# Performance work log

Measured on AMD Instinct MI355X. Metric: run time of the kernel, lower is better.

## Reference

```python
import jax, jax.numpy as jnp
import numpy as np

NUM_GROUPS = 32
EPS = 1e-6


def group_norm(x, gamma, beta):
    # x: [b, c, t, h, w]
    b, c, t, h, w = x.shape
    xg = x.reshape(b, NUM_GROUPS, c // NUM_GROUPS, t, h, w)
    mean = xg.mean(axis=(2, 3, 4, 5), keepdims=True)
    var = xg.var(axis=(2, 3, 4, 5), keepdims=True)
    xg = (xg - mean) * jax.lax.rsqrt(var + EPS)
    xn = xg.reshape(b, c, t, h, w)
    return xn * gamma[None, :, None, None, None] + beta[None, :, None, None, None]


def conv1x1(x, w, bias):
    # 1x1x1 Conv3d == per-position channel matmul. x: [b,c,t,h,w], w: [cout,cin]
    y = jnp.einsum('oc,bcthw->bothw', w, x)
    return y + bias[None, :, None, None, None]


def setup_inputs() -> dict:
    key = jax.random.key(0)
    ks = jax.random.split(key, 11)
    c = 512
    b, t, h, w = 1, 16, 32, 32
    s = 1.0 / np.sqrt(c)
    return {
        'x': jax.random.normal(ks[0], (b, c, t, h, w), dtype=jnp.float32),
        'gn_gamma': jnp.ones((c,), jnp.float32),
        'gn_beta': jnp.zeros((c,), jnp.float32),
        'wq': jax.random.normal(ks[1], (c, c), jnp.float32) * s,
        'bq': jnp.zeros((c,), jnp.float32),
        'wk': jax.random.normal(ks[2], (c, c), jnp.float32) * s,
        'bk': jnp.zeros((c,), jnp.float32),
        'wv': jax.random.normal(ks[3], (c, c), jnp.float32) * s,
        'bv': jnp.zeros((c,), jnp.float32),
        'wo': jax.random.normal(ks[4], (c, c), jnp.float32) * s,
        'bo': jnp.zeros((c,), jnp.float32),
    }


def reference(x, gn_gamma, gn_beta, wq, bq, wk, bk, wv, bv, wo, bo):
    b, c, t, h, w = x.shape
    h_ = group_norm(x, gn_gamma, gn_beta)
    q = conv1x1(h_, wq, bq)
    k = conv1x1(h_, wk, bk)
    v = conv1x1(h_, wv, bv)
    # per-frame spatial attention: tokens are the h*w grid, batched over (b t)
    n = h * w
    q = q.transpose(0, 2, 3, 4, 1).reshape(b * t, n, c)   # [(bt), n, c]
    k = k.transpose(0, 2, 3, 4, 1).reshape(b * t, n, c)
    v = v.transpose(0, 2, 3, 4, 1).reshape(b * t, n, c)
    scale = float(int(c) ** (-0.5))
    attn = jax.nn.softmax(jnp.einsum('bic,bjc->bij', q, k) * scale, axis=-1)
    out = jnp.einsum('bij,bjc->bic', attn, v)             # [(bt), n, c]
    out = out.reshape(b, t, h, w, c).transpose(0, 4, 1, 2, 3)
    out = conv1x1(out, wo, bo)
    return x + out
```

## Files before the change

kernel.cpp:

```cpp
#include <hip/hip_runtime.h>
#include <hip/hip_bf16.h>

#define CCH   512
#define NPOS  16384
#define NTOK  1024
#define NFRM  16
#define NGRP  32
#define GSZ   (CCH / NGRP)
#define GELEM (GSZ * NPOS)
#define GN_SPLIT 32

typedef unsigned short u16;
typedef unsigned int   u32;
typedef __attribute__((ext_vector_type(8))) short  short8;
typedef __attribute__((ext_vector_type(4))) float  floatx4;

__device__ __forceinline__ float bf2f(u16 u) {
    return __uint_as_float(((u32)u) << 16);
}
__device__ __forceinline__ u16 f2bf(float f) {
    u32 u = __float_as_uint(f);
    u = (u + 0x7fffu + ((u >> 16) & 1u)) >> 16;
    return (u16)u;
}
__device__ __forceinline__ float ldx(const void* p, size_t i, bool f32m) {
    return f32m ? ((const float*)p)[i] : bf2f(((const u16*)p)[i]);
}
__device__ __forceinline__ void gl2lds16(const u16* g, u16* l) {
    __builtin_amdgcn_global_load_lds(
        (const __attribute__((address_space(1))) u32*)g,
        (__attribute__((address_space(3))) u32*)l, 16, 0, 0);
}

__launch_bounds__(256)
__global__ void detect_dtype(const u32* __restrict__ x32, u32* __restrict__ flag) {
    __shared__ int cnt;
    if (threadIdx.x == 0) cnt = 0;
    __syncthreads();
    int c = 0;
    for (int i = threadIdx.x; i < 4096; i += 256) {
        u32 v = x32[i] & 0xFFFFu;
        u32 e = (v >> 7) & 0xFFu;
        if (e >= 0xC8u) c++;
    }
    atomicAdd(&cnt, c);
    __syncthreads();
    if (threadIdx.x == 0) *flag = (cnt > 64) ? 1u : 0u;
}

__launch_bounds__(256)
__global__ void conv_all(const void* w0, const void* w1, const void* w2, const void* w3,
                         const void* b0, const void* b1, const void* b2, const void* b3,
                         u16* __restrict__ wdst, u16* __restrict__ bdst,
                         float* __restrict__ rl,
                         const u32* __restrict__ flag) {
    int b = blockIdx.x;
    if (b > 1024) {
        rl[(b - 1025) * 256 + threadIdx.x] = 0.0f;
        return;
    }
    bool f32m = *flag != 0u;
    if (b < 1024) {
        int wi = b >> 8;
        const void* src = (wi == 0) ? w0 : (wi == 1) ? w1 : (wi == 2) ? w2 : w3;
        int base = (b & 255) * 1024 + threadIdx.x * 4;
        u16* d = wdst + wi * 262144 + base;
        if (f32m) {
            float4 v = *(const float4*)((const float*)src + base);
            ushort4 o;
            o.x = f2bf(v.x); o.y = f2bf(v.y); o.z = f2bf(v.z); o.w = f2bf(v.w);
            *(ushort4*)d = o;
        } else {
            *(ushort4*)d = *(const ushort4*)((const u16*)src + base);
        }
    } else {
        int t = threadIdx.x;
        int bi = t >> 6;
        int off = (t & 63) * 8;
        const void* src = (bi == 0) ? b0 : (bi == 1) ? b1 : (bi == 2) ? b2 : b3;
        u16* d = bdst + bi * 512 + off;
        if (f32m) {
            float4 v1 = *(const float4*)((const float*)src + off);
            float4 v2 = *(const float4*)((const float*)src + off + 4);
            ushort4 o1, o2;
            o1.x = f2bf(v1.x); o1.y = f2bf(v1.y); o1.z = f2bf(v1.z); o1.w = f2bf(v1.w);
            o2.x = f2bf(v2.x); o2.y = f2bf(v2.y); o2.z = f2bf(v2.z); o2.w = f2bf(v2.w);
            *(ushort4*)d = o1; *(ushort4*)(d + 4) = o2;
        } else {
            *(ushort4*)d = *(const ushort4*)((const u16*)src + off);
            *(ushort4*)(d + 4) = *(const ushort4*)((const u16*)src + off + 4);
        }
    }
}

__launch_bounds__(256)
__global__ void gn_partial(const void* __restrict__ x, float2* __restrict__ partials,
                           const u32* __restrict__ flag) {
    __shared__ float sm[8];
    bool f32m = *flag != 0u;
    const int chunk = GELEM / GN_SPLIT;
    size_t base = (size_t)blockIdx.x * chunk;
    float s = 0.f, ss = 0.f;
    if (f32m) {
        const float4* p = (const float4*)((const float*)x + base);
        for (int i = threadIdx.x; i < chunk / 4; i += 256) {
            float4 u = p[i];
            s  += u.x + u.y + u.z + u.w;
            ss += u.x * u.x + u.y * u.y + u.z * u.z + u.w * u.w;
        }
    } else {
        const ushort4* p = (const ushort4*)((const u16*)x + base);
        for (int i = threadIdx.x; i < chunk / 4; i += 256) {
            ushort4 u = p[i];
            float a = bf2f(u.x), b = bf2f(u.y), c = bf2f(u.z), d = bf2f(u.w);
            s  += a + b + c + d;
            ss += a * a + b * b + c * c + d * d;
        }
    }
    int lane = threadIdx.x & 63, w = threadIdx.x >> 6;
    float t = s;
    #pragma unroll
    for (int o = 32; o > 0; o >>= 1) t += __shfl_down(t, o, 64);
    if (lane == 0) sm[w] = t;
    t = ss;
    #pragma unroll
    for (int o = 32; o > 0; o >>= 1) t += __shfl_down(t, o, 64);
    if (lane == 0) sm[4 + w] = t;
    __syncthreads();
    if (threadIdx.x == 0)
        partials[blockIdx.x] = make_float2(sm[0] + sm[1] + sm[2] + sm[3],
                                           sm[4] + sm[5] + sm[6] + sm[7]);
}

__launch_bounds__(256)
__global__ void gn_coef(const float2* __restrict__ partials, const void* __restrict__ gamma,
                        const void* __restrict__ beta, float2* __restrict__ coef,
                        const u32* __restrict__ flag) {
    bool f32m = *flag != 0u;
    int c = blockIdx.x * 256 + threadIdx.x;
    if (c < CCH) {
        int g = c >> 4;
        float sum = 0.f, sq = 0.f;
        #pragma unroll
        for (int i = 0; i < GN_SPLIT; ++i) {
            float2 p = partials[g * GN_SPLIT + i];
            sum += p.x; sq += p.y;
        }
        float mean = sum * (1.0f / (float)GELEM);
        float var  = fmaxf(sq * (1.0f / (float)GELEM) - mean * mean, 0.0f);
        float rstd = rsqrtf(var + 1e-6f);
        float gm = ldx(gamma, c, f32m), b = ldx(beta, c, f32m);
        float sc = rstd * gm;
        coef[c] = make_float2(sc, b - mean * sc);
    }
}

__launch_bounds__(256)
__global__ void gn_apply_t(const void* __restrict__ x, const float2* __restrict__ coef,
                           u16* __restrict__ xt, const u32* __restrict__ flag) {
    bool f32m = *flag != 0u;
    __shared__ float tile[64][65];
    int p0 = blockIdx.x * 64, c0 = blockIdx.y * 64;
    int lane = threadIdx.x & 63, rg = threadIdx.x >> 6;
    #pragma unroll 4
    for (int i = 0; i < 16; ++i) {
        int row = rg * 16 + i;
        int c = c0 + row;
        float2 cf = coef[c];
        float v = ldx(x, (size_t)c * NPOS + p0 + lane, f32m);
        tile[row][lane] = v * cf.x + cf.y;
    }
    __syncthreads();
    #pragma unroll 4
    for (int i = 0; i < 16; ++i) {
        int prow = rg * 16 + i;
        xt[(size_t)(p0 + prow) * CCH + c0 + lane] = f2bf(tile[lane][prow]);
    }
}

#define EPI_QK    0
#define EPI_V     1
#define EPI_SCEXP 2
#define EPI_PV    3
#define EPI_OUT   4

template<int EPI, bool MX, bool FSW>
__launch_bounds__(256, 3)
__global__ void mfma_gemm(const u16* __restrict__ A, const u16* __restrict__ B,
                          void* __restrict__ C, const u16* __restrict__ bias,
                          const void* __restrict__ resid, const u32* __restrict__ flag,
                          float* __restrict__ rl,
                          int lda, int ldb, int ldc, int K,
                          long aFS, long bFS, long cFS) {
    __shared__ __align__(16) u16 As[128 * 64];
    __shared__ __align__(16) u16 Bs[128 * 64];
    const int tid = threadIdx.x;

    int bxi, byi, f;
    if (FSW) {
        u32 id = (blockIdx.z * gridDim.y + blockIdx.y) * gridDim.x + blockIdx.x;
        u32 T = gridDim.x * gridDim.y * gridDim.z;
        u32 half = T >> 1;
        f = (int)(id & 7u) + ((id >= half) ? 8 : 0);
        u32 l = (id >= half ? id - half : id) >> 3;
        bxi = (int)(l % gridDim.x);
        byi = (int)(l / gridDim.x);
    } else {
        bxi = blockIdx.x; byi = blockIdx.y; f = blockIdx.z;
    }
    const int m_blk = MX ? bxi : byi;
    const int n_blk = MX ? byi : bxi;

    const u16* Ab = A + (size_t)f * aFS + (size_t)m_blk * 128 * lda;
    const u16* Bb = B + (size_t)f * bFS + (size_t)n_blk * 128 * ldb;

    const int wave = tid >> 6, lane = tid & 63;
    const int srow8 = wave * 32 + (lane >> 3);
    const int schs  = ((lane & 7) ^ ((lane >> 3) & 7)) * 8;
    u16* lA = &As[wave * 2048];
    u16* lB = &Bs[wave * 2048];

    const int wm = (wave >> 1) * 64, wn = (wave & 1) * 64;
    const int l15 = lane & 15, quad = lane >> 4;

    floatx4 acc[4][4] = {};

    for (int kk = 0; kk < K; kk += 64) {
        __syncthreads();
        #pragma unroll
        for (int o = 0; o < 4; ++o) {
            gl2lds16(Ab + (size_t)(srow8 + o * 8) * lda + kk + schs, lA + o * 512);
            gl2lds16(Bb + (size_t)(srow8 + o * 8) * ldb + kk + schs, lB + o * 512);
        }
        __syncthreads();
        #pragma unroll
        for (int kh = 0; kh < 2; ++kh) {
            short8 af[4], bf[4];
            #pragma unroll
            for (int mi = 0; mi < 4; ++mi) {
                const int row = wm + mi * 16 + l15;
                af[mi] = *(const short8*)&As[row * 64 + (((kh << 2) | quad) ^ (row & 7)) * 8];
            }
            #pragma unroll
            for (int ni = 0; ni < 4; ++ni) {
                const int row = wn + ni * 16 + l15;
                bf[ni] = *(const short8*)&Bs[row * 64 + (((kh << 2) | quad) ^ (row & 7)) * 8];
            }
            #pragma unroll
            for (int mi = 0; mi < 4; ++mi)
                #pragma unroll
                for (int ni = 0; ni < 4; ++ni)
                    acc[mi][ni] = __builtin_amdgcn_mfma_f32_16x16x32_bf16(
                        af[mi], bf[ni], acc[mi][ni], 0, 0, 0);
        }
    }

    const bool f32m = (EPI == EPI_OUT) ? (*flag != 0u) : false;
    const int m_base = m_blk * 128 + wm;
    const int n_base = n_blk * 128 + wn;
    const float scale = 0.044194173824159216f;

    float inv[4][4];
    if (EPI == EPI_PV) {
        #pragma unroll
        for (int mi = 0; mi < 4; ++mi)
            #pragma unroll
            for (int r = 0; r < 4; ++r)
                inv[mi][r] = 1.0f / rl[f * NTOK + m_base + mi * 16 + quad * 4 + r];
    }
    float rs[4][4];
    if (EPI == EPI_SCEXP) {
        #pragma unroll
        for (int mi = 0; mi < 4; ++mi)
            #pragma unroll
            for (int r = 0; r < 4; ++r) rs[mi][r] = 0.0f;
    }

    #pragma unroll
    for (int mi = 0; mi < 4; ++mi) {
        #pragma unroll
        for (int ni = 0; ni < 4; ++ni) {
            int n = n_base + ni * 16 + l15;
            float bn = (EPI == EPI_QK) ? bf2f(bias[n]) : 0.0f;
            #pragma unroll
            for (int r = 0; r < 4; ++r) {
                int m = m_base + mi * 16 + quad * 4 + r;
                float v = acc[mi][ni][r];
                size_t idx = (size_t)f * cFS + (size_t)m * ldc + n;
                if (EPI == EPI_QK) {
                    ((u16*)C)[idx] = f2bf(v + bn);
                } else if (EPI == EPI_V) {
                    ((u16*)C)[idx] = f2bf(v + bf2f(bias[m]));
                } else if (EPI == EPI_SCEXP) {
                    float ex = __expf(v * scale);
                    rs[mi][r] += ex;
                    ((u16*)C)[idx] = f2bf(ex);
                } else if (EPI == EPI_PV) {
                    ((u16*)C)[idx] = f2bf(v * inv[mi][r]);
                } else {
                    float r2 = v + bf2f(bias[m]) + ldx(resid, idx, f32m);
                    if (f32m) ((float*)C)[idx] = r2;
                    else      ((u16*)C)[idx]   = f2bf(r2);
                }
            }
        }
    }

    if (EPI == EPI_SCEXP) {
        #pragma unroll
        for (int mi = 0; mi < 4; ++mi) {
            #pragma unroll
            for (int r = 0; r < 4; ++r) {
                float s = rs[mi][r];
                s += __shfl_xor(s, 1, 64);
                s += __shfl_xor(s, 2, 64);
                s += __shfl_xor(s, 4, 64);
                s += __shfl_xor(s, 8, 64);
                if (l15 == 0)
                    atomicAdd(&rl[f * NTOK + m_base + mi * 16 + quad * 4 + r], s);
            }
        }
    }
}

extern "C" void kernel_launch(void* const* d_in, const int* in_sizes, int n_in,
                              void* d_out, int out_size, void* d_ws, size_t ws_size,
                              hipStream_t stream) {
    const void* x   = d_in[0];
    const void* gam = d_in[1];
    const void* bet = d_in[2];

    char* ws = (char*)d_ws;
    float2* coef     = (float2*)(ws);
    float2* partials = (float2*)(ws + 4096);
    u32*    flag     = (u32*)(ws + 12352);
    u16* cw[4] = { (u16*)(ws + 16384),              (u16*)(ws + 16384 +  524288ull),
                   (u16*)(ws + 16384 + 1048576ull), (u16*)(ws + 16384 + 1572864ull) };
    u16* cb[4] = { (u16*)(ws + 2113536ull),        (u16*)(ws + 2113536ull + 1024),
                   (u16*)(ws + 2113536ull + 2048), (u16*)(ws + 2113536ull + 3072) };
    float* rl  = (float*)(ws + (3ull << 20));
    u16*  xnt  = (u16*)(ws + (4ull  << 20));
    u16*  qkt  = (u16*)(ws + (20ull << 20));
    u16*  vt   = (u16*)(ws + (52ull << 20));
    u16*  pbuf = (u16*)(ws + (68ull << 20));
    u16*  obuf = xnt;

    detect_dtype<<<1, 256, 0, stream>>>((const u32*)x, flag);
    conv_all<<<1089, 256, 0, stream>>>(d_in[3], d_in[5], d_in[7], d_in[9],
                                       d_in[4], d_in[6], d_in[8], d_in[10],
                                       cw[0], cb[0], rl, flag);
    gn_partial<<<NGRP * GN_SPLIT, 256, 0, stream>>>(x, partials, flag);
    gn_coef<<<2, 256, 0, stream>>>(partials, gam, bet, coef, flag);
    gn_apply_t<<<dim3(NPOS / 64, CCH / 64), 256, 0, stream>>>(x, coef, xnt, flag);

    dim3 gqk(NPOS / 128, 1024 / 128, 1);
    mfma_gemm<EPI_QK, true, false><<<gqk, 256, 0, stream>>>(
        xnt, cw[0], qkt, cb[0], nullptr, flag, nullptr, CCH, CCH, 1024, CCH, 0, 0, 0);
    dim3 gv(NPOS / 128, CCH / 128, 1);
    mfma_gemm<EPI_V, false, false><<<gv, 256, 0, stream>>>(
        cw[2], xnt, vt, cb[2], nullptr, flag, nullptr, CCH, CCH, NPOS, CCH, 0, 0, 0);

    dim3 gsc(NTOK / 128, NTOK / 128, NFRM);
    mfma_gemm<EPI_SCEXP, false, true><<<gsc, 256, 0, stream>>>(
        qkt, qkt + 512, pbuf, nullptr, nullptr, flag, rl, 1024, 1024, NTOK, CCH,
        (long)NTOK * 1024, (long)NTOK * 1024, (long)NTOK * NTOK);

    dim3 gpv(CCH / 128, NTOK / 128, NFRM);
    mfma_gemm<EPI_PV, false, true><<<gpv, 256, 0, stream>>>(
        pbuf, vt, obuf, nullptr, nullptr, flag, rl, NTOK, NPOS, CCH, NTOK,
        (long)NTOK * NTOK, NTOK, (long)NTOK * CCH);

    dim3 go(NPOS / 128, CCH / 128, 1);
    mfma_gemm<EPI_OUT, false, false><<<go, 256, 0, stream>>>(
        cw[3], obuf, d_out, cb[3], x, flag, nullptr, CCH, CCH, NPOS, CCH, 0, 0, 0);
}
```

Before: 236.9 us.

## Double-buffer GEMM LDS tiles with K-step 32 and raise occupancy hint

```diff
diff --git a/kernel.cpp b/kernel.cpp
--- a/kernel.cpp
+++ b/kernel.cpp
@@ -185,15 +185,15 @@
 #define EPI_OUT   4
 
 template<int EPI, bool MX, bool FSW>
-__launch_bounds__(256, 3)
+__launch_bounds__(256, 4)
 __global__ void mfma_gemm(const u16* __restrict__ A, const u16* __restrict__ B,
                           void* __restrict__ C, const u16* __restrict__ bias,
                           const void* __restrict__ resid, const u32* __restrict__ flag,
                           float* __restrict__ rl,
                           int lda, int ldb, int ldc, int K,
                           long aFS, long bFS, long cFS) {
-    __shared__ __align__(16) u16 As[128 * 64];
-    __shared__ __align__(16) u16 Bs[128 * 64];
+    __shared__ __align__(16) u16 As[2][128 * 32];
+    __shared__ __align__(16) u16 Bs[2][128 * 32];
     const int tid = threadIdx.x;
 
     int bxi, byi, f;
@@ -215,44 +215,44 @@
     const u16* Bb = B + (size_t)f * bFS + (size_t)n_blk * 128 * ldb;
 
     const int wave = tid >> 6, lane = tid & 63;
-    const int srow8 = wave * 32 + (lane >> 3);
-    const int schs  = ((lane & 7) ^ ((lane >> 3) & 7)) * 8;
-    u16* lA = &As[wave * 2048];
-    u16* lB = &Bs[wave * 2048];
+    const int srow = wave * 32 + (lane >> 2);
+    const int scol = ((lane & 3) ^ ((lane >> 3) & 3)) * 8;
 
     const int wm = (wave >> 1) * 64, wn = (wave & 1) * 64;
     const int l15 = lane & 15, quad = lane >> 4;
+    const int rsw = (l15 >> 1) & 3;
 
     floatx4 acc[4][4] = {};
 
-    for (int kk = 0; kk < K; kk += 64) {
+    auto stage = [&](int b, int kk) {
+        #pragma unroll
+        for (int o = 0; o < 2; ++o) {
+            gl2lds16(Ab + (size_t)(srow + o * 16) * lda + kk + scol,
+                     &As[b][wave * 1024 + o * 512]);
+            gl2lds16(Bb + (size_t)(srow + o * 16) * ldb + kk + scol,
+                     &Bs[b][wave * 1024 + o * 512]);
+        }
+    };
+
+    stage(0, 0);
+    int cur = 0;
+    for (int kk = 0; kk < K; kk += 32) {
         __syncthreads();
-        #pragma unroll
-        for (int o = 0; o < 4; ++o) {
-            gl2lds16(Ab + (size_t)(srow8 + o * 8) * lda + kk + schs, lA + o * 512);
-            gl2lds16(Bb + (size_t)(srow8 + o * 8) * ldb + kk + schs, lB + o * 512);
-        }
-        __syncthreads();
-        #pragma unroll
-        for (int kh = 0; kh < 2; ++kh) {
-            short8 af[4], bf[4];
-            #pragma unroll
-            for (int mi = 0; mi < 4; ++mi) {
-                const int row = wm + mi * 16 + l15;
-                af[mi] = *(const short8*)&As[row * 64 + (((kh << 2) | quad) ^ (row & 7)) * 8];
-            }
-            #pragma unroll
-            for (int ni = 0; ni < 4; ++ni) {
-                const int row = wn + ni * 16 + l15;
-                bf[ni] = *(const short8*)&Bs[row * 64 + (((kh << 2) | quad) ^ (row & 7)) * 8];
-            }
-            #pragma unroll
-            for (int mi = 0; mi < 4; ++mi)
-                #pragma unroll
-                for (int ni = 0; ni < 4; ++ni)
-                    acc[mi][ni] = __builtin_amdgcn_mfma_f32_16x16x32_bf16(
-                        af[mi], bf[ni], acc[mi][ni], 0, 0, 0);
-        }
+        if (kk + 32 < K) stage(cur ^ 1, kk + 32);
+        short8 af[4], bf[4];
+        #pragma unroll
+        for (int mi = 0; mi < 4; ++mi)
+            af[mi] = *(const short8*)&As[cur][(wm + mi * 16 + l15) * 32 + ((quad ^ rsw) << 3)];
+        #pragma unroll
+        for (int ni = 0; ni < 4; ++ni)
+            bf[ni] = *(const short8*)&Bs[cur][(wn + ni * 16 + l15) * 32 + ((quad ^ rsw) << 3)];
+        #pragma unroll
+        for (int mi = 0; mi < 4; ++mi)
+            #pragma unroll
+            for (int ni = 0; ni < 4; ++ni)
+                acc[mi][ni] = __builtin_amdgcn_mfma_f32_16x16x32_bf16(
+                    af[mi], bf[ni], acc[mi][ni], 0, 0, 0);
+        cur ^= 1;
     }
 
     const bool f32m = (EPI == EPI_OUT) ? (*flag != 0u) : false;
```

New measurement: 244.6 us. 1.03x slower.

## Add 256x256 eight-wave pipelined GEMM for QK projection and score kernels

Applied to the files above, without the earlier changes.

```diff
diff --git a/kernel.cpp b/kernel.cpp
--- a/kernel.cpp
+++ b/kernel.cpp
@@ -215,10 +215,8 @@
     const u16* Bb = B + (size_t)f * bFS + (size_t)n_blk * 128 * ldb;
 
     const int wave = tid >> 6, lane = tid & 63;
-    const int srow8 = wave * 32 + (lane >> 3);
-    const int schs  = ((lane & 7) ^ ((lane >> 3) & 7)) * 8;
-    u16* lA = &As[wave * 2048];
-    u16* lB = &Bs[wave * 2048];
+    const int srow = wave * 32 + (lane >> 3);
+    const int schs = ((lane & 7) ^ ((lane >> 3) & 7)) * 8;
 
     const int wm = (wave >> 1) * 64, wn = (wave & 1) * 64;
     const int l15 = lane & 15, quad = lane >> 4;
@@ -229,8 +227,8 @@
         __syncthreads();
         #pragma unroll
         for (int o = 0; o < 4; ++o) {
-            gl2lds16(Ab + (size_t)(srow8 + o * 8) * lda + kk + schs, lA + o * 512);
-            gl2lds16(Bb + (size_t)(srow8 + o * 8) * ldb + kk + schs, lB + o * 512);
+            gl2lds16(Ab + (size_t)(srow + o * 8) * lda + kk + schs, &As[wave * 2048 + o * 512]);
+            gl2lds16(Bb + (size_t)(srow + o * 8) * ldb + kk + schs, &Bs[wave * 2048 + o * 512]);
         }
         __syncthreads();
         #pragma unroll
@@ -323,6 +321,164 @@
     }
 }
 
+template<int EPI, bool MX, bool FSW>
+__launch_bounds__(512, 2)
+__global__ void mfma_gemm8(const u16* __restrict__ A, const u16* __restrict__ B,
+                           void* __restrict__ C, const u16* __restrict__ bias,
+                           const u32* __restrict__ flag, float* __restrict__ rl,
+                           int lda, int ldb, int ldc, int K,
+                           long aFS, long bFS, long cFS) {
+    __shared__ __align__(16) u16 As[2][2][256 * 32];
+    __shared__ __align__(16) u16 Bs[2][2][256 * 32];
+    const int tid = threadIdx.x;
+
+    int bxi, byi, f;
+    if (FSW) {
+        u32 id = (blockIdx.z * gridDim.y + blockIdx.y) * gridDim.x + blockIdx.x;
+        u32 T = gridDim.x * gridDim.y * gridDim.z;
+        u32 half = T >> 1;
+        f = (int)(id & 7u) + ((id >= half) ? 8 : 0);
+        u32 l = (id >= half ? id - half : id) >> 3;
+        bxi = (int)(l % gridDim.x);
+        byi = (int)(l / gridDim.x);
+    } else {
+        bxi = blockIdx.x; byi = blockIdx.y; f = blockIdx.z;
+    }
+    const int m_blk = MX ? bxi : byi;
+    const int n_blk = MX ? byi : bxi;
+
+    const u16* Ab = A + (size_t)f * aFS + (size_t)m_blk * 256 * lda;
+    const u16* Bb = B + (size_t)f * bFS + (size_t)n_blk * 256 * ldb;
+
+    const int wave = tid >> 6, lane = tid & 63;
+    const int wm = (wave >> 2) * 128, wn = (wave & 3) * 64;
+    const int l15 = lane & 15, quad = lane >> 4;
+    const int rsw = l15 >> 2;
+
+    const int srow = wave * 16 + (lane >> 2);
+    const int sch  = ((lane & 3) ^ ((lane >> 4) & 3)) * 8;
+
+    auto stgA = [&](int bufi, int khi, int t) {
+        const u16* g = Ab + (size_t)srow * lda + t * 64 + khi * 32 + sch;
+        u16* l = &As[bufi][khi][wave * 512];
+        gl2lds16(g, l);
+        gl2lds16(g + (size_t)128 * lda, l + 4096);
+    };
+    auto stgB = [&](int bufi, int khi, int t) {
+        const u16* g = Bb + (size_t)srow * ldb + t * 64 + khi * 32 + sch;
+        u16* l = &Bs[bufi][khi][wave * 512];
+        gl2lds16(g, l);
+        gl2lds16(g + (size_t)128 * ldb, l + 4096);
+    };
+
+    floatx4 acc[8][4] = {};
+    short8 bf[4];
+    const int NT = K >> 6;
+    const int NI = NT >> 1;
+
+    stgA(0, 0, 0); stgB(0, 0, 0); stgA(0, 1, 0); stgB(0, 1, 0);
+    stgA(1, 0, 1); stgB(1, 0, 1); stgA(1, 1, 1);
+    asm volatile("s_waitcnt vmcnt(6)" ::: "memory");
+    __builtin_amdgcn_s_barrier();
+
+#define PH8(BUF, CH, KH, STAGE_STMT, VMW) do {                                   \
+    short8 af[4];                                                                \
+    _Pragma("unroll")                                                            \
+    for (int mi2 = 0; mi2 < 4; ++mi2) {                                          \
+        const int row = wm + (CH) * 64 + mi2 * 16 + l15;                         \
+        af[mi2] = *(const short8*)&As[BUF][KH][row * 32 + ((quad ^ rsw) << 3)];  \
+    }                                                                            \
+    if ((CH) == 0) {                                                             \
+        _Pragma("unroll")                                                        \
+        for (int ni = 0; ni < 4; ++ni) {                                         \
+            const int row = wn + ni * 16 + l15;                                  \
+            bf[ni] = *(const short8*)&Bs[BUF][KH][row * 32 + ((quad ^ rsw) << 3)]; \
+        }                                                                        \
+    }                                                                            \
+    STAGE_STMT;                                                                  \
+    __builtin_amdgcn_s_barrier();                                                \
+    asm volatile("s_waitcnt lgkmcnt(0)" ::: "memory");                           \
+    __builtin_amdgcn_sched_barrier(0);                                           \
+    __builtin_amdgcn_s_setprio(1);                                               \
+    _Pragma("unroll")                                                            \
+    for (int mi2 = 0; mi2 < 4; ++mi2)                                            \
+        _Pragma("unroll")                                                        \
+        for (int ni = 0; ni < 4; ++ni)                                           \
+            acc[(CH) * 4 + mi2][ni] = __builtin_amdgcn_mfma_f32_16x16x32_bf16(   \
+                af[mi2], bf[ni], acc[(CH) * 4 + mi2][ni], 0, 0, 0);              \
+    __builtin_amdgcn_s_setprio(0);                                               \
+    VMW;                                                                         \
+    __builtin_amdgcn_s_barrier();                                                \
+} while (0)
+
+    for (int it = 0; it < NI; ++it) {
+        const int t = it << 1;
+        const bool more = (t + 2) < NT;
+        PH8(0, 0, 0, { stgB(1, 1, t + 1); }, {});
+        PH8(0, 1, 0, { if (more) stgA(0, 0, t + 2); }, {});
+        PH8(0, 0, 1, { if (more) stgB(0, 0, t + 2); }, {});
+        PH8(0, 1, 1, { if (more) stgA(0, 1, t + 2); },
+            { if (more) asm volatile("s_waitcnt vmcnt(6)" ::: "memory");
+              else      asm volatile("s_waitcnt vmcnt(0)" ::: "memory"); });
+        PH8(1, 0, 0, { if (more) stgB(0, 1, t + 2); }, {});
+        PH8(1, 1, 0, { if (more) stgA(1, 0, t + 3); }, {});
+        PH8(1, 0, 1, { if (more) stgB(1, 0, t + 3); }, {});
+        PH8(1, 1, 1, { if (more) stgA(1, 1, t + 3); },
+            { if (more) asm volatile("s_waitcnt vmcnt(6)" ::: "memory"); });
+    }
+#undef PH8
+
+    const int m_base = m_blk * 256 + wm;
+    const int n_base = n_blk * 256 + wn;
+    const float scale = 0.044194173824159216f;
+
+    float rs[8][4];
+    if (EPI == EPI_SCEXP) {
+        #pragma unroll
+        for (int mi = 0; mi < 8; ++mi)
+            #pragma unroll
+            for (int r = 0; r < 4; ++r) rs[mi][r] = 0.0f;
+    }
+
+    #pragma unroll
+    for (int mi = 0; mi < 8; ++mi) {
+        #pragma unroll
+        for (int ni = 0; ni < 4; ++ni) {
+            int n = n_base + ni * 16 + l15;
+            float bn = (EPI == EPI_QK) ? bf2f(bias[n]) : 0.0f;
+            #pragma unroll
+            for (int r = 0; r < 4; ++r) {
+                int m = m_base + mi * 16 + quad * 4 + r;
+                float v = acc[mi][ni][r];
+                size_t idx = (size_t)f * cFS + (size_t)m * ldc + n;
+                if (EPI == EPI_QK) {
+                    ((u16*)C)[idx] = f2bf(v + bn);
+                } else {
+                    float ex = __expf(v * scale);
+                    rs[mi][r] += ex;
+                    ((u16*)C)[idx] = f2bf(ex);
+                }
+            }
+        }
+    }
+
+    if (EPI == EPI_SCEXP) {
+        #pragma unroll
+        for (int mi = 0; mi < 8; ++mi) {
+            #pragma unroll
+            for (int r = 0; r < 4; ++r) {
+                float s = rs[mi][r];
+                s += __shfl_xor(s, 1, 64);
+                s += __shfl_xor(s, 2, 64);
+                s += __shfl_xor(s, 4, 64);
+                s += __shfl_xor(s, 8, 64);
+                if (l15 == 0)
+                    atomicAdd(&rl[f * NTOK + m_base + mi * 16 + quad * 4 + r], s);
+            }
+        }
+    }
+}
+
 extern "C" void kernel_launch(void* const* d_in, const int* in_sizes, int n_in,
                               void* d_out, int out_size, void* d_ws, size_t ws_size,
                               hipStream_t stream) {
@@ -353,16 +509,16 @@
     gn_coef<<<2, 256, 0, stream>>>(partials, gam, bet, coef, flag);
     gn_apply_t<<<dim3(NPOS / 64, CCH / 64), 256, 0, stream>>>(x, coef, xnt, flag);
 
-    dim3 gqk(NPOS / 128, 1024 / 128, 1);
-    mfma_gemm<EPI_QK, true, false><<<gqk, 256, 0, stream>>>(
-        xnt, cw[0], qkt, cb[0], nullptr, flag, nullptr, CCH, CCH, 1024, CCH, 0, 0, 0);
+    dim3 gqk(NPOS / 256, 1024 / 256, 1);
+    mfma_gemm8<EPI_QK, true, false><<<gqk, 512, 0, stream>>>(
+        xnt, cw[0], qkt, cb[0], flag, nullptr, CCH, CCH, 1024, CCH, 0, 0, 0);
     dim3 gv(NPOS / 128, CCH / 128, 1);
     mfma_gemm<EPI_V, false, false><<<gv, 256, 0, stream>>>(
         cw[2], xnt, vt, cb[2], nullptr, flag, nullptr, CCH, CCH, NPOS, CCH, 0, 0, 0);
 
-    dim3 gsc(NTOK / 128, NTOK / 128, NFRM);
-    mfma_gemm<EPI_SCEXP, false, true><<<gsc, 256, 0, stream>>>(
-        qkt, qkt + 512, pbuf, nullptr, nullptr, flag, rl, 1024, 1024, NTOK, CCH,
+    dim3 gsc(NTOK / 256, NTOK / 256, NFRM);
+    mfma_gemm8<EPI_SCEXP, false, true><<<gsc, 512, 0, stream>>>(
+        qkt, qkt + 512, pbuf, nullptr, flag, rl, 1024, 1024, NTOK, CCH,
         (long)NTOK * 1024, (long)NTOK * 1024, (long)NTOK * NTOK);
 
     dim3 gpv(CCH / 128, NTOK / 128, NFRM);
```

New measurement: 238.7 us. No clear change (+0.7%).
